# Kernel optimization log

Hardware: AMD Instinct MI355X
Metric: run time of the kernel (lower is better)

The kernel has to match this reference:

```python
import jax, jax.numpy as jnp
import numpy as np

VOX_X, VOX_Y, VOX_Z = 256, 256, 20   # ceil((pc_range[3:]-pc_range[:3]) / 0.4)
OUT_H, OUT_W, OUT_Z = 200, 200, 16   # hard-coded F.interpolate target in forward
C = 80                               # out_channels; sparse feat dim must match for concat
N_PTS = 200000
BS = 1
EPS = 1e-5


def _lin_interp(x, axis, out_size):
    """1D linear interp along `axis`, matching torch align_corners=False."""
    in_size = x.shape[axis]
    pos = (jnp.arange(out_size, dtype=jnp.float32) + 0.5) * (in_size / out_size) - 0.5
    pos = jnp.clip(pos, 0.0, in_size - 1)
    i0 = jnp.floor(pos).astype(jnp.int32)
    i1 = jnp.minimum(i0 + 1, in_size - 1)
    w = pos - i0.astype(jnp.float32)
    x0 = jnp.take(x, i0, axis=axis)
    x1 = jnp.take(x, i1, axis=axis)
    wshape = [1] * x.ndim
    wshape[axis] = out_size
    w = w.reshape(wshape)
    return x0 * (1.0 - w) + x1 * w


def setup_inputs() -> dict:
    key = jax.random.key(0)
    ks = jax.random.split(key, 8)
    bev_feats = jax.random.normal(ks[0], (BS, C, OUT_H, OUT_W, OUT_Z), dtype=jnp.float32)
    # coords: [batch_idx, x, y, z] with per-column valid ranges
    cb = jax.random.randint(ks[1], (N_PTS, 1), 0, BS, dtype=jnp.int32)
    cx = jax.random.randint(ks[2], (N_PTS, 1), 0, VOX_X, dtype=jnp.int32)
    cy = jax.random.randint(ks[3], (N_PTS, 1), 0, VOX_Y, dtype=jnp.int32)
    cz = jax.random.randint(ks[4], (N_PTS, 1), 0, VOX_Z, dtype=jnp.int32)
    coords = jnp.concatenate([cb, cx, cy, cz], axis=1)
    feats = jax.random.normal(ks[5], (N_PTS, C), dtype=jnp.float32)
    w_conv = jax.random.normal(ks[6], (C, 2 * C), dtype=jnp.float32) * (1.0 / np.sqrt(2 * C))
    b_conv = jnp.zeros((C,), dtype=jnp.float32)
    return {
        "bev_feats": bev_feats, "coords": coords, "feats": feats,
        "w_conv": w_conv, "b_conv": b_conv,
        "bn_gamma": jnp.ones((C,), jnp.float32), "bn_beta": jnp.zeros((C,), jnp.float32),
        "bn_mean": jnp.zeros((C,), jnp.float32), "bn_var": jnp.ones((C,), jnp.float32),
    }


def reference(bev_feats, coords, feats, w_conv, b_conv, bn_gamma, bn_beta, bn_mean, bn_var):
    bs = bev_feats.shape[0]
    voxel = jnp.zeros((bs, VOX_X, VOX_Y, VOX_Z, C), dtype=jnp.float32)
    voxel = voxel.at[coords[:, 0], coords[:, 1], coords[:, 2], coords[:, 3]].set(feats)
    # permute(0,4,2,1,3): (bs, X, Y, Z, C) -> (bs, C, Y, X, Z)
    prior = jnp.transpose(voxel, (0, 4, 2, 1, 3))
    # trilinear interpolate (256,256,20) -> (200,200,16), align_corners=False (separable)
    prior = _lin_interp(prior, 2, OUT_H)
    prior = _lin_interp(prior, 3, OUT_W)
    prior = _lin_interp(prior, 4, OUT_Z)
    # concat on channels -> 1x1x1 conv3d -> BN (eval stats) -> residual -> ReLU
    x = jnp.concatenate([bev_feats, prior], axis=1)  # (bs, 2C, H, W, Z)
    y = jnp.einsum('bchwz,oc->bohwz', x, w_conv) + b_conv[None, :, None, None, None]
    inv = bn_gamma * jax.lax.rsqrt(bn_var + EPS)
    y = y * inv[None, :, None, None, None] + (bn_beta - bn_mean * inv)[None, :, None, None, None]
    return jax.nn.relu(y + bev_feats)
```

## Files before the change

kernel.cpp:

```cpp
#include <hip/hip_runtime.h>
#include <hip/hip_bf16.h>

#define VXX 256
#define VYY 256
#define VZZ 20
#define NC  80
#define OH  200
#define OW  200
#define OZ  16
#define SPATIAL (OH*OW*OZ)
#define NVOX (VXX*VYY*VZZ)
#define EPSV 1e-5f
#define NS 64
#define NWG (SPATIAL/NS)
#define X_FOOT 6
#define NCELL (2*X_FOOT*VZZ)
#define SLOTS 48
#define PSTR 72
#define RSB 80
#define RSP 88

typedef float  f32x4 __attribute__((ext_vector_type(4)));
typedef short  s16x8 __attribute__((ext_vector_type(8)));

__device__ __forceinline__ ushort f2bf(float f) {
    uint u = __builtin_bit_cast(uint, f);
    u += 0x7FFFu + ((u >> 16) & 1u);
    return (ushort)(u >> 16);
}

__device__ __forceinline__ void bar_lgkm() {
    asm volatile("s_waitcnt lgkmcnt(0)" ::: "memory");
    __builtin_amdgcn_s_barrier();
    asm volatile("" ::: "memory");
}

__global__ void scatter_k(const int* __restrict__ coords, int npts,
                          int* __restrict__ winner) {
    int i = blockIdx.x * 256 + threadIdx.x;
    if (i >= npts) return;
    int b = coords[i*4+0];
    int x = coords[i*4+1];
    int y = coords[i*4+2];
    int z = coords[i*4+3];
    int vi = ((b*VXX + x)*VYY + y)*VZZ + z;
    atomicMax(&winner[vi], i);
}

__global__ void setup_k(const float* __restrict__ wconv,
                        const float* __restrict__ bconv,
                        const float* __restrict__ gamma,
                        const float* __restrict__ beta,
                        const float* __restrict__ mean,
                        const float* __restrict__ var,
                        int4* __restrict__ winner4,
                        ushort* __restrict__ wfrag,
                        float2* __restrict__ bnss) {
    const int b = blockIdx.x, tid = threadIdx.x;
    if (b < 1280) {
        winner4[b*256 + tid] = make_int4(-1, -1, -1, -1);
    } else if (b < 1330) {
        int idx = (b - 1280)*256 + tid;
        int f   = idx >> 9;
        int rem = idx & 511;
        int l   = rem >> 3;
        int j   = rem & 7;
        int mt  = f / 5;
        int ks  = f - mt*5;
        int o   = mt*16 + (l & 15);
        int c   = ks*32 + (l >> 4)*8 + j;
        wfrag[idx] = f2bf(wconv[o*160 + c]);
    } else if (tid < NC) {
        float inv = gamma[tid] * rsqrtf(var[tid] + EPSV);
        bnss[tid] = make_float2(inv, bconv[tid]*inv + beta[tid] - mean[tid]*inv);
    }
}

__launch_bounds__(256, 5)
__global__ void fused_k(const float* __restrict__ bev,
                        const float* __restrict__ feats,
                        const int*  __restrict__ winner,
                        const ushort* __restrict__ wfrag,
                        const float2* __restrict__ bnss,
                        float* __restrict__ out) {
    __shared__ __align__(16) ushort xb_lds[NS * RSB];
    __shared__ __align__(16) char   u_lds[20736];
    __shared__ int    idx_lds[NCELL];
    __shared__ int    slot_pi[SLOTS];
    __shared__ int    wavecnt[4];
    ushort* const P_lds  = (ushort*)u_lds;
    ushort* const Rt_lds = (ushort*)(u_lds + 9216);
    ushort* const xp_lds = (ushort*)u_lds;

    const int tid   = threadIdx.x;
    const int bid   = blockIdx.x;
    const int swzb  = (bid & 7) * (NWG/8) + (bid >> 3);
    const int sbase = swzb * NS;
    const int sl    = tid & 63;
    const int quarter = tid >> 6;
    const int wv    = quarter, lane = sl;

    const int h  = sbase / (OW * OZ);
    const int w0 = (sbase >> 4) % OW;
    float posy = (h + 0.5f) * ((float)VYY/(float)OH) - 0.5f;
    posy = fminf(fmaxf(posy, 0.f), (float)(VYY-1));
    const int   y0 = (int)posy;
    const int   y1 = min(y0+1, VYY-1);
    const float fy = posy - (float)y0;
    float posx0 = (w0 + 0.5f) * ((float)VXX/(float)OW) - 0.5f;
    posx0 = fminf(fmaxf(posx0, 0.f), (float)(VXX-1));
    const int xmin = (int)posx0;

    const int zq = sl & 15;
    const int wq = w0 + (sl >> 4);
    float posx = (wq + 0.5f) * ((float)VXX/(float)OW) - 0.5f;
    posx = fminf(fmaxf(posx, 0.f), (float)(VXX-1));
    const int   x0 = (int)posx;
    const int   x1 = min(x0+1, VXX-1);
    const float fxw = posx - (float)x0;
    float posz = (zq + 0.5f) * ((float)VZZ/(float)OZ) - 0.5f;
    posz = fminf(fmaxf(posz, 0.f), (float)(VZZ-1));
    const int   z0 = (int)posz;
    const int   z1 = min(z0+1, VZZ-1);
    const float fzw = posz - (float)z0;
    const int fx0 = x0 - xmin, fx1 = x1 - xmin;

    int pi = -1;
    if (tid < NCELL) {
        int fz  = tid % VZZ;
        int fx  = (tid / VZZ) % X_FOOT;
        int fyc = tid / (VZZ * X_FOOT);
        int xx  = min(xmin + fx, VXX-1);
        int yy  = fyc ? y1 : y0;
        pi = winner[(xx*VYY + yy)*VZZ + fz];
    }
    __builtin_amdgcn_sched_barrier(0);

    const int S = sbase + sl;
    float bvv[20];
    #pragma unroll
    for (int j = 0; j < 20; ++j)
        bvv[j] = bev[(quarter*20 + j)*SPATIAL + S];
    __builtin_amdgcn_sched_barrier(0);

    {
        uint* pz = (uint*)u_lds;
        #pragma unroll
        for (int i = 0; i < 9; ++i) pz[tid + i*256] = 0;
    }

    unsigned long long bm = __ballot(pi >= 0);
    if (lane == 0) wavecnt[wv] = __popcll(bm);
    bar_lgkm();
    int base = 0, nstot = 0;
    #pragma unroll
    for (int w2 = 0; w2 < 4; ++w2) {
        int c2 = wavecnt[w2];
        if (w2 < wv) base += c2;
        nstot += c2;
    }
    if (tid < NCELL) {
        int v = -1;
        if (pi >= 0) {
            int slot = base + __popcll(bm & ((1ull << lane) - 1ull));
            if (slot < SLOTS) { slot_pi[slot] = pi; v = slot; }
            else v = -(pi + 2);
        }
        idx_lds[tid] = v;
    }
    bar_lgkm();
    const int nst = min(nstot, SLOTS);

    const float4* feats4 = (const float4*)feats;
    const int myslot = tid >> 2, part = tid & 3;
    const bool rowact = (myslot < nst);
    float4 rbuf[5];
    if (rowact) {
        const float4* p = feats4 + slot_pi[myslot]*20 + part*5;
        #pragma unroll
        for (int q = 0; q < 5; ++q) rbuf[q] = p[q];
    }

    {
        const int ky = quarter >> 1, kx = quarter & 1;
        const float ywp = ky ? fy : 1.f - fy;
        const bool xdup = (fx1 == fx0);
        if (!(xdup && kx)) {
            const int   xf = kx ? fx1 : fx0;
            const float xw = xdup ? 1.f : (kx ? fxw : 1.f - fxw);
            #pragma unroll
            for (int kz = 0; kz < 2; ++kz) {
                int cell = (ky*X_FOOT + xf)*VZZ + (kz ? z1 : z0);
                int v = idx_lds[cell];
                if (v >= 0)
                    P_lds[sl*PSTR + v] = f2bf(ywp * xw * (kz ? fzw : 1.f - fzw));
            }
        }
    }

    #pragma unroll
    for (int j5 = 0; j5 < 5; ++j5) {
        ushort4 pk = make_ushort4(f2bf(bvv[j5*4+0]), f2bf(bvv[j5*4+1]),
                                  f2bf(bvv[j5*4+2]), f2bf(bvv[j5*4+3]));
        *(ushort4*)&xb_lds[sl*RSB + quarter*20 + j5*4] = pk;
    }

    {
        ushort vals[20];
        #pragma unroll
        for (int q = 0; q < 5; ++q) {
            vals[4*q+0] = rowact ? f2bf(rbuf[q].x) : (ushort)0;
            vals[4*q+1] = rowact ? f2bf(rbuf[q].y) : (ushort)0;
            vals[4*q+2] = rowact ? f2bf(rbuf[q].z) : (ushort)0;
            vals[4*q+3] = rowact ? f2bf(rbuf[q].w) : (ushort)0;
        }
        #pragma unroll
        for (int e = 0; e < 20; ++e)
            Rt_lds[(part*20 + e)*PSTR + myslot] = vals[e];
    }
    bar_lgkm();

    const int lrow = lane & 15, lgrp = lane >> 4;
    f32x4 pa[5];
    {
        const int prow = (wv*16 + lrow)*PSTR;
        s16x8 p0 = *(const s16x8*)&P_lds[prow +      lgrp*8];
        s16x8 p1 = *(const s16x8*)&P_lds[prow + 32 + lgrp*8];
        #pragma unroll
        for (int mt = 0; mt < 5; ++mt) {
            const int arow = (mt*16 + lrow)*PSTR;
            s16x8 a0 = *(const s16x8*)&Rt_lds[arow +      lgrp*8];
            s16x8 a1 = *(const s16x8*)&Rt_lds[arow + 32 + lgrp*8];
            pa[mt] = (f32x4){0.f, 0.f, 0.f, 0.f};
            pa[mt] = __builtin_amdgcn_mfma_f32_16x16x32_bf16(a0, p0, pa[mt], 0, 0, 0);
            pa[mt] = __builtin_amdgcn_mfma_f32_16x16x32_bf16(a1, p1, pa[mt], 0, 0, 0);
        }
    }
    bar_lgkm();
    #pragma unroll
    for (int mt = 0; mt < 5; ++mt) {
        ushort4 pk = make_ushort4(f2bf(pa[mt][0]), f2bf(pa[mt][1]),
                                  f2bf(pa[mt][2]), f2bf(pa[mt][3]));
        *(ushort4*)&xp_lds[(wv*16 + lrow)*RSP + mt*16 + lgrp*4] = pk;
    }

    if (nstot > SLOTS) {
        bar_lgkm();
        float add20[20];
        #pragma unroll
        for (int j = 0; j < 20; ++j) add20[j] = 0.f;
        bool any = false;
        #pragma unroll
        for (int k = 0; k < 8; ++k) {
            int kz = k & 1, kx = (k>>1)&1, ky = k>>2;
            int cell = (ky*X_FOOT + (kx ? fx1 : fx0))*VZZ + (kz ? z1 : z0);
            int v = idx_lds[cell];
            if (v < -1) {
                any = true;
                float wtk = (ky?fy:1.f-fy) * (kx?fxw:1.f-fxw) * (kz?fzw:1.f-fzw);
                const float4* p = feats4 + (-v - 2)*20 + quarter*5;
                #pragma unroll
                for (int q = 0; q < 5; ++q) {
                    float4 f = p[q];
                    add20[4*q]   += wtk*f.x; add20[4*q+1] += wtk*f.y;
                    add20[4*q+2] += wtk*f.z; add20[4*q+3] += wtk*f.w;
                }
            }
        }
        if (any) {
            #pragma unroll
            for (int q = 0; q < 5; ++q) {
                ushort* dst = &xp_lds[sl*RSP + quarter*20 + q*4];
                ushort4 old = *(ushort4*)dst;
                const ushort ov[4] = {old.x, old.y, old.z, old.w};
                ushort nv[4];
                #pragma unroll
                for (int e = 0; e < 4; ++e) {
                    float f = __builtin_bit_cast(float, (uint)ov[e] << 16) + add20[4*q+e];
                    nv[e] = f2bf(f);
                }
                *(ushort4*)dst = make_ushort4(nv[0], nv[1], nv[2], nv[3]);
            }
        }
    }
    bar_lgkm();

    f32x4 acc[5];
    #pragma unroll
    for (int mt = 0; mt < 5; ++mt) acc[mt] = (f32x4){0.f, 0.f, 0.f, 0.f};

    const int srow_b = (wv*16 + lrow) * RSB;
    const int srow_p = (wv*16 + lrow) * RSP;

    #pragma unroll
    for (int ks = 0; ks < 5; ++ks) {
        int c = ks*32 + lgrp*8;
        const ushort* bp = (c < 80) ? &xb_lds[srow_b + c]
                                    : &xp_lds[srow_p + (c - 80)];
        s16x8 b = *(const s16x8*)bp;
        #pragma unroll
        for (int mt = 0; mt < 5; ++mt) {
            s16x8 a = *(const s16x8*)&wfrag[((mt*5 + ks)*64 + lane)*8];
            acc[mt] = __builtin_amdgcn_mfma_f32_16x16x32_bf16(a, b, acc[mt], 0, 0, 0);
        }
    }

    const int slocal = wv*16 + lrow;
    const int sglob  = sbase + slocal;
    #pragma unroll
    for (int mt = 0; mt < 5; ++mt) {
        ushort4 rr = *(const ushort4*)&xb_lds[slocal*RSB + mt*16 + lgrp*4];
        const ushort rrv[4] = {rr.x, rr.y, rr.z, rr.w};
        #pragma unroll
        for (int r = 0; r < 4; ++r) {
            int o = mt*16 + lgrp*4 + r;
            float2 ss = bnss[o];
            float resid = __builtin_bit_cast(float, (uint)rrv[r] << 16);
            float v = acc[mt][r]*ss.x + ss.y + resid;
            out[o*SPATIAL + sglob] = fmaxf(v, 0.f);
        }
    }
}

extern "C" void kernel_launch(void* const* d_in, const int* in_sizes, int n_in,
                              void* d_out, int out_size, void* d_ws, size_t ws_size,
                              hipStream_t stream) {
    const float* bev    = (const float*)d_in[0];
    const int*   coords = (const int*)  d_in[1];
    const float* feats  = (const float*)d_in[2];
    const float* wconv  = (const float*)d_in[3];
    const float* bconv  = (const float*)d_in[4];
    const float* gamma  = (const float*)d_in[5];
    const float* beta   = (const float*)d_in[6];
    const float* mean   = (const float*)d_in[7];
    const float* var    = (const float*)d_in[8];
    float*       out    = (float*)d_out;

    int*    winner = (int*)d_ws;
    ushort* wfrag  = (ushort*)((char*)d_ws + (size_t)NVOX*4);
    float2* bnss   = (float2*)((char*)d_ws + (size_t)NVOX*4 + 25600);
    int npts = in_sizes[1] / 4;

    hipLaunchKernelGGL(setup_k, dim3(1331), dim3(256), 0, stream,
                       wconv, bconv, gamma, beta, mean, var,
                       (int4*)winner, wfrag, bnss);
    hipLaunchKernelGGL(scatter_k, dim3((npts + 255)/256), dim3(256), 0, stream,
                       coords, npts, winner);
    hipLaunchKernelGGL(fused_k, dim3(NWG), dim3(256), 0, stream,
                       bev, feats, winner, wfrag, bnss, out);
}
```

Measured before the change: 151.2 us.

## Make fused kernel persistent over 5 tiles with software-prefetched loads

The fused kernel now launches 2000 blocks, each looping over 5 consecutive 64-voxel tiles, instead of one tile per block. The next tile's winner indices and bev values are loaded into registers while the current tile's conv MFMAs and stores proceed, to hide global load latency and amortise per-block setup. The cost is more live registers, which may reduce occupancy under the 5-wave launch bound, and fewer blocks to spread across CUs, leaving some tail imbalance.

```diff
diff --git a/kernel.cpp b/kernel.cpp
--- a/kernel.cpp
+++ b/kernel.cpp
@@ -12,7 +12,8 @@
 #define NVOX (VXX*VYY*VZZ)
 #define EPSV 1e-5f
 #define NS 64
-#define NWG (SPATIAL/NS)
+#define NT 5
+#define NB 2000
 #define X_FOOT 6
 #define NCELL (2*X_FOOT*VZZ)
 #define SLOTS 48
@@ -92,232 +93,271 @@
     ushort* const Rt_lds = (ushort*)(u_lds + 9216);
     ushort* const xp_lds = (ushort*)u_lds;
 
-    const int tid   = threadIdx.x;
-    const int bid   = blockIdx.x;
-    const int swzb  = (bid & 7) * (NWG/8) + (bid >> 3);
-    const int sbase = swzb * NS;
-    const int sl    = tid & 63;
+    const int tid  = threadIdx.x;
+    const int sl   = tid & 63;
     const int quarter = tid >> 6;
-    const int wv    = quarter, lane = sl;
-
-    const int h  = sbase / (OW * OZ);
-    const int w0 = (sbase >> 4) % OW;
+    const int wv   = quarter, lane = sl;
+    const int lrow = lane & 15, lgrp = lane >> 4;
+
+    const int bid      = blockIdx.x;
+    const int xcd      = bid & 7, rank = bid >> 3;
+    const int tilebase = xcd*(NB/8*NT) + rank*NT;
+
+    const int h   = tilebase / 50;
+    const int w0b = (tilebase % 50) * 4;
+    const float XS = (float)VXX / (float)OW;
+
     float posy = (h + 0.5f) * ((float)VYY/(float)OH) - 0.5f;
     posy = fminf(fmaxf(posy, 0.f), (float)(VYY-1));
     const int   y0 = (int)posy;
     const int   y1 = min(y0+1, VYY-1);
     const float fy = posy - (float)y0;
-    float posx0 = (w0 + 0.5f) * ((float)VXX/(float)OW) - 0.5f;
-    posx0 = fminf(fmaxf(posx0, 0.f), (float)(VXX-1));
-    const int xmin = (int)posx0;
 
     const int zq = sl & 15;
-    const int wq = w0 + (sl >> 4);
-    float posx = (wq + 0.5f) * ((float)VXX/(float)OW) - 0.5f;
-    posx = fminf(fmaxf(posx, 0.f), (float)(VXX-1));
-    const int   x0 = (int)posx;
-    const int   x1 = min(x0+1, VXX-1);
-    const float fxw = posx - (float)x0;
     float posz = (zq + 0.5f) * ((float)VZZ/(float)OZ) - 0.5f;
     posz = fminf(fmaxf(posz, 0.f), (float)(VZZ-1));
     const int   z0 = (int)posz;
     const int   z1 = min(z0+1, VZZ-1);
     const float fzw = posz - (float)z0;
-    const int fx0 = x0 - xmin, fx1 = x1 - xmin;
-
-    int pi = -1;
-    if (tid < NCELL) {
-        int fz  = tid % VZZ;
-        int fx  = (tid / VZZ) % X_FOOT;
-        int fyc = tid / (VZZ * X_FOOT);
-        int xx  = min(xmin + fx, VXX-1);
-        int yy  = fyc ? y1 : y0;
-        pi = winner[(xx*VYY + yy)*VZZ + fz];
+
+    const int dfz  = tid % VZZ;
+    const int dfx  = (tid / VZZ) % X_FOOT;
+    const int dfyc = tid / (VZZ * X_FOOT);
+    const int dyy  = dfyc ? y1 : y0;
+
+    const float4* feats4 = (const float4*)feats;
+
+    int   pi = -1;
+    float bvv[20];
+    {
+        float px0 = (w0b + 0.5f)*XS - 0.5f;
+        px0 = fminf(fmaxf(px0, 0.f), (float)(VXX-1));
+        int xmin0 = (int)px0;
+        if (tid < NCELL) {
+            int xx = min(xmin0 + dfx, VXX-1);
+            pi = winner[(xx*VYY + dyy)*VZZ + dfz];
+        }
     }
     __builtin_amdgcn_sched_barrier(0);
-
-    const int S = sbase + sl;
-    float bvv[20];
-    #pragma unroll
-    for (int j = 0; j < 20; ++j)
-        bvv[j] = bev[(quarter*20 + j)*SPATIAL + S];
+    {
+        int S0 = tilebase*NS + sl;
+        #pragma unroll
+        for (int j = 0; j < 20; ++j)
+            bvv[j] = bev[(quarter*20 + j)*SPATIAL + S0];
+    }
     __builtin_amdgcn_sched_barrier(0);
-
     {
         uint* pz = (uint*)u_lds;
         #pragma unroll
         for (int i = 0; i < 9; ++i) pz[tid + i*256] = 0;
     }
 
-    unsigned long long bm = __ballot(pi >= 0);
-    if (lane == 0) wavecnt[wv] = __popcll(bm);
-    bar_lgkm();
-    int base = 0, nstot = 0;
     #pragma unroll
-    for (int w2 = 0; w2 < 4; ++w2) {
-        int c2 = wavecnt[w2];
-        if (w2 < wv) base += c2;
-        nstot += c2;
-    }
-    if (tid < NCELL) {
-        int v = -1;
-        if (pi >= 0) {
-            int slot = base + __popcll(bm & ((1ull << lane) - 1ull));
-            if (slot < SLOTS) { slot_pi[slot] = pi; v = slot; }
-            else v = -(pi + 2);
-        }
-        idx_lds[tid] = v;
-    }
-    bar_lgkm();
-    const int nst = min(nstot, SLOTS);
-
-    const float4* feats4 = (const float4*)feats;
-    const int myslot = tid >> 2, part = tid & 3;
-    const bool rowact = (myslot < nst);
-    float4 rbuf[5];
-    if (rowact) {
-        const float4* p = feats4 + slot_pi[myslot]*20 + part*5;
-        #pragma unroll
-        for (int q = 0; q < 5; ++q) rbuf[q] = p[q];
-    }
-
-    {
-        const int ky = quarter >> 1, kx = quarter & 1;
-        const float ywp = ky ? fy : 1.f - fy;
-        const bool xdup = (fx1 == fx0);
-        if (!(xdup && kx)) {
-            const int   xf = kx ? fx1 : fx0;
-            const float xw = xdup ? 1.f : (kx ? fxw : 1.f - fxw);
-            #pragma unroll
-            for (int kz = 0; kz < 2; ++kz) {
-                int cell = (ky*X_FOOT + xf)*VZZ + (kz ? z1 : z0);
+    for (int t = 0; t < NT; ++t) {
+        const int tile  = tilebase + t;
+        const int sbase = tile * NS;
+        const int w0    = w0b + 4*t;
+
+        float posx = (w0 + (sl >> 4) + 0.5f)*XS - 0.5f;
+        posx = fminf(fmaxf(posx, 0.f), (float)(VXX-1));
+        const int   x0 = (int)posx;
+        const int   x1 = min(x0+1, VXX-1);
+        const float fxw = posx - (float)x0;
+        float px0 = (w0 + 0.5f)*XS - 0.5f;
+        px0 = fminf(fmaxf(px0, 0.f), (float)(VXX-1));
+        const int xmin = (int)px0;
+        const int fx0 = x0 - xmin, fx1 = x1 - xmin;
+
+        unsigned long long bm = __ballot(pi >= 0);
+        if (lane == 0) wavecnt[wv] = __popcll(bm);
+        bar_lgkm();
+        int base = 0, nstot = 0;
+        #pragma unroll
+        for (int w2 = 0; w2 < 4; ++w2) {
+            int c2 = wavecnt[w2];
+            if (w2 < wv) base += c2;
+            nstot += c2;
+        }
+        if (tid < NCELL) {
+            int v = -1;
+            if (pi >= 0) {
+                int slot = base + __popcll(bm & ((1ull << lane) - 1ull));
+                if (slot < SLOTS) { slot_pi[slot] = pi; v = slot; }
+                else v = -(pi + 2);
+            }
+            idx_lds[tid] = v;
+        }
+        bar_lgkm();
+        const int nst = min(nstot, SLOTS);
+
+        const int myslot = tid >> 2, part = tid & 3;
+        const bool rowact = (myslot < nst);
+        float4 rbuf[5];
+        if (rowact) {
+            const float4* p = feats4 + slot_pi[myslot]*20 + part*5;
+            #pragma unroll
+            for (int q = 0; q < 5; ++q) rbuf[q] = p[q];
+        }
+
+        {
+            const int ky = quarter >> 1, kx = quarter & 1;
+            const float ywp = ky ? fy : 1.f - fy;
+            const bool xdup = (fx1 == fx0);
+            if (!(xdup && kx)) {
+                const int   xf = kx ? fx1 : fx0;
+                const float xw = xdup ? 1.f : (kx ? fxw : 1.f - fxw);
+                #pragma unroll
+                for (int kz = 0; kz < 2; ++kz) {
+                    int cell = (ky*X_FOOT + xf)*VZZ + (kz ? z1 : z0);
+                    int v = idx_lds[cell];
+                    if (v >= 0)
+                        P_lds[sl*PSTR + v] = f2bf(ywp * xw * (kz ? fzw : 1.f - fzw));
+                }
+            }
+        }
+
+        #pragma unroll
+        for (int j5 = 0; j5 < 5; ++j5) {
+            ushort4 pk = make_ushort4(f2bf(bvv[j5*4+0]), f2bf(bvv[j5*4+1]),
+                                      f2bf(bvv[j5*4+2]), f2bf(bvv[j5*4+3]));
+            *(ushort4*)&xb_lds[sl*RSB + quarter*20 + j5*4] = pk;
+        }
+
+        {
+            ushort vals[20];
+            #pragma unroll
+            for (int q = 0; q < 5; ++q) {
+                vals[4*q+0] = rowact ? f2bf(rbuf[q].x) : (ushort)0;
+                vals[4*q+1] = rowact ? f2bf(rbuf[q].y) : (ushort)0;
+                vals[4*q+2] = rowact ? f2bf(rbuf[q].z) : (ushort)0;
+                vals[4*q+3] = rowact ? f2bf(rbuf[q].w) : (ushort)0;
+            }
+            #pragma unroll
+            for (int e = 0; e < 20; ++e)
+                Rt_lds[(part*20 + e)*PSTR + myslot] = vals[e];
+        }
+        bar_lgkm();
+
+        f32x4 pa[5];
+        {
+            const int prow = (wv*16 + lrow)*PSTR;
+            s16x8 p0 = *(const s16x8*)&P_lds[prow +      lgrp*8];
+            s16x8 p1 = *(const s16x8*)&P_lds[prow + 32 + lgrp*8];
+            #pragma unroll
+            for (int mt = 0; mt < 5; ++mt) {
+                const int arow = (mt*16 + lrow)*PSTR;
+                s16x8 a0 = *(const s16x8*)&Rt_lds[arow +      lgrp*8];
+                s16x8 a1 = *(const s16x8*)&Rt_lds[arow + 32 + lgrp*8];
+                pa[mt] = (f32x4){0.f, 0.f, 0.f, 0.f};
+                pa[mt] = __builtin_amdgcn_mfma_f32_16x16x32_bf16(a0, p0, pa[mt], 0, 0, 0);
+                pa[mt] = __builtin_amdgcn_mfma_f32_16x16x32_bf16(a1, p1, pa[mt], 0, 0, 0);
+            }
+        }
+        bar_lgkm();
+        #pragma unroll
+        for (int mt = 0; mt < 5; ++mt) {
+            ushort4 pk = make_ushort4(f2bf(pa[mt][0]), f2bf(pa[mt][1]),
+                                      f2bf(pa[mt][2]), f2bf(pa[mt][3]));
+            *(ushort4*)&xp_lds[(wv*16 + lrow)*RSP + mt*16 + lgrp*4] = pk;
+        }
+
+        if (t + 1 < NT) {
+            float px0n = (w0 + 4 + 0.5f)*XS - 0.5f;
+            px0n = fminf(fmaxf(px0n, 0.f), (float)(VXX-1));
+            int xminN = (int)px0n;
+            pi = -1;
+            if (tid < NCELL) {
+                int xx = min(xminN + dfx, VXX-1);
+                pi = winner[(xx*VYY + dyy)*VZZ + dfz];
+            }
+            int Sn = (tile + 1)*NS + sl;
+            #pragma unroll
+            for (int j = 0; j < 20; ++j)
+                bvv[j] = bev[(quarter*20 + j)*SPATIAL + Sn];
+            __builtin_amdgcn_sched_barrier(0);
+        }
+
+        if (nstot > SLOTS) {
+            bar_lgkm();
+            float add20[20];
+            #pragma unroll
+            for (int j = 0; j < 20; ++j) add20[j] = 0.f;
+            bool any = false;
+            #pragma unroll
+            for (int k = 0; k < 8; ++k) {
+                int kz = k & 1, kx = (k>>1)&1, ky = k>>2;
+                int cell = (ky*X_FOOT + (kx ? fx1 : fx0))*VZZ + (kz ? z1 : z0);
                 int v = idx_lds[cell];
-                if (v >= 0)
-                    P_lds[sl*PSTR + v] = f2bf(ywp * xw * (kz ? fzw : 1.f - fzw));
-            }
-        }
-    }
-
-    #pragma unroll
-    for (int j5 = 0; j5 < 5; ++j5) {
-        ushort4 pk = make_ushort4(f2bf(bvv[j5*4+0]), f2bf(bvv[j5*4+1]),
-                                  f2bf(bvv[j5*4+2]), f2bf(bvv[j5*4+3]));
-        *(ushort4*)&xb_lds[sl*RSB + quarter*20 + j5*4] = pk;
-    }
-
-    {
-        ushort vals[20];
-        #pragma unroll
-        for (int q = 0; q < 5; ++q) {
-            vals[4*q+0] = rowact ? f2bf(rbuf[q].x) : (ushort)0;
-            vals[4*q+1] = rowact ? f2bf(rbuf[q].y) : (ushort)0;
-            vals[4*q+2] = rowact ? f2bf(rbuf[q].z) : (ushort)0;
-            vals[4*q+3] = rowact ? f2bf(rbuf[q].w) : (ushort)0;
-        }
-        #pragma unroll
-        for (int e = 0; e < 20; ++e)
-            Rt_lds[(part*20 + e)*PSTR + myslot] = vals[e];
-    }
-    bar_lgkm();
-
-    const int lrow = lane & 15, lgrp = lane >> 4;
-    f32x4 pa[5];
-    {
-        const int prow = (wv*16 + lrow)*PSTR;
-        s16x8 p0 = *(const s16x8*)&P_lds[prow +      lgrp*8];
-        s16x8 p1 = *(const s16x8*)&P_lds[prow + 32 + lgrp*8];
-        #pragma unroll
-        for (int mt = 0; mt < 5; ++mt) {
-            const int arow = (mt*16 + lrow)*PSTR;
-            s16x8 a0 = *(const s16x8*)&Rt_lds[arow +      lgrp*8];
-            s16x8 a1 = *(const s16x8*)&Rt_lds[arow + 32 + lgrp*8];
-            pa[mt] = (f32x4){0.f, 0.f, 0.f, 0.f};
-            pa[mt] = __builtin_amdgcn_mfma_f32_16x16x32_bf16(a0, p0, pa[mt], 0, 0, 0);
-            pa[mt] = __builtin_amdgcn_mfma_f32_16x16x32_bf16(a1, p1, pa[mt], 0, 0, 0);
-        }
-    }
-    bar_lgkm();
-    #pragma unroll
-    for (int mt = 0; mt < 5; ++mt) {
-        ushort4 pk = make_ushort4(f2bf(pa[mt][0]), f2bf(pa[mt][1]),
-                                  f2bf(pa[mt][2]), f2bf(pa[mt][3]));
-        *(ushort4*)&xp_lds[(wv*16 + lrow)*RSP + mt*16 + lgrp*4] = pk;
-    }
-
-    if (nstot > SLOTS) {
-        bar_lgkm();
-        float add20[20];
-        #pragma unroll
-        for (int j = 0; j < 20; ++j) add20[j] = 0.f;
-        bool any = false;
-        #pragma unroll
-        for (int k = 0; k < 8; ++k) {
-            int kz = k & 1, kx = (k>>1)&1, ky = k>>2;
-            int cell = (ky*X_FOOT + (kx ? fx1 : fx0))*VZZ + (kz ? z1 : z0);
-            int v = idx_lds[cell];
-            if (v < -1) {
-                any = true;
-                float wtk = (ky?fy:1.f-fy) * (kx?fxw:1.f-fxw) * (kz?fzw:1.f-fzw);
-                const float4* p = feats4 + (-v - 2)*20 + quarter*5;
+                if (v < -1) {
+                    any = true;
+                    float wtk = (ky?fy:1.f-fy) * (kx?fxw:1.f-fxw) * (kz?fzw:1.f-fzw);
+                    const float4* p = feats4 + (-v - 2)*20 + quarter*5;
+                    #pragma unroll
+                    for (int q = 0; q < 5; ++q) {
+                        float4 f = p[q];
+                        add20[4*q]   += wtk*f.x; add20[4*q+1] += wtk*f.y;
+                        add20[4*q+2] += wtk*f.z; add20[4*q+3] += wtk*f.w;
+                    }
+                }
+            }
+            if (any) {
                 #pragma unroll
                 for (int q = 0; q < 5; ++q) {
-                    float4 f = p[q];
-                    add20[4*q]   += wtk*f.x; add20[4*q+1] += wtk*f.y;
-                    add20[4*q+2] += wtk*f.z; add20[4*q+3] += wtk*f.w;
+                    ushort* dst = &xp_lds[sl*RSP + quarter*20 + q*4];
+                    ushort4 old = *(ushort4*)dst;
+                    const ushort ov[4] = {old.x, old.y, old.z, old.w};
+                    ushort nv[4];
+                    #pragma unroll
+                    for (int e = 0; e < 4; ++e) {
+                        float f = __builtin_bit_cast(float, (uint)ov[e] << 16) + add20[4*q+e];
+                        nv[e] = f2bf(f);
+                    }
+                    *(ushort4*)dst = make_ushort4(nv[0], nv[1], nv[2], nv[3]);
                 }
             }
         }
-        if (any) {
-            #pragma unroll
-            for (int q = 0; q < 5; ++q) {
-                ushort* dst = &xp_lds[sl*RSP + quarter*20 + q*4];
-                ushort4 old = *(ushort4*)dst;
-                const ushort ov[4] = {old.x, old.y, old.z, old.w};
-                ushort nv[4];
-                #pragma unroll
-                for (int e = 0; e < 4; ++e) {
-                    float f = __builtin_bit_cast(float, (uint)ov[e] << 16) + add20[4*q+e];
-                    nv[e] = f2bf(f);
-                }
-                *(ushort4*)dst = make_ushort4(nv[0], nv[1], nv[2], nv[3]);
-            }
-        }
-    }
-    bar_lgkm();
-
-    f32x4 acc[5];
-    #pragma unroll
-    for (int mt = 0; mt < 5; ++mt) acc[mt] = (f32x4){0.f, 0.f, 0.f, 0.f};
-
-    const int srow_b = (wv*16 + lrow) * RSB;
-    const int srow_p = (wv*16 + lrow) * RSP;
-
-    #pragma unroll
-    for (int ks = 0; ks < 5; ++ks) {
-        int c = ks*32 + lgrp*8;
-        const ushort* bp = (c < 80) ? &xb_lds[srow_b + c]
-                                    : &xp_lds[srow_p + (c - 80)];
-        s16x8 b = *(const s16x8*)bp;
+        bar_lgkm();
+
+        f32x4 acc[5];
+        #pragma unroll
+        for (int mt = 0; mt < 5; ++mt) acc[mt] = (f32x4){0.f, 0.f, 0.f, 0.f};
+
+        const int srow_b = (wv*16 + lrow) * RSB;
+        const int srow_p = (wv*16 + lrow) * RSP;
+
+        #pragma unroll
+        for (int ks = 0; ks < 5; ++ks) {
+            int c = ks*32 + lgrp*8;
+            const ushort* bp = (c < 80) ? &xb_lds[srow_b + c]
+                                        : &xp_lds[srow_p + (c - 80)];
+            s16x8 b = *(const s16x8*)bp;
+            #pragma unroll
+            for (int mt = 0; mt < 5; ++mt) {
+                s16x8 a = *(const s16x8*)&wfrag[((mt*5 + ks)*64 + lane)*8];
+                acc[mt] = __builtin_amdgcn_mfma_f32_16x16x32_bf16(a, b, acc[mt], 0, 0, 0);
+            }
+        }
+        bar_lgkm();
+
+        if (t + 1 < NT) {
+            uint* pz = (uint*)u_lds;
+            #pragma unroll
+            for (int i = 0; i < 9; ++i) pz[tid + i*256] = 0;
+        }
+        const int slocal = wv*16 + lrow;
+        const int sglob  = sbase + slocal;
         #pragma unroll
         for (int mt = 0; mt < 5; ++mt) {
-            s16x8 a = *(const s16x8*)&wfrag[((mt*5 + ks)*64 + lane)*8];
-            acc[mt] = __builtin_amdgcn_mfma_f32_16x16x32_bf16(a, b, acc[mt], 0, 0, 0);
-        }
-    }
-
-    const int slocal = wv*16 + lrow;
-    const int sglob  = sbase + slocal;
-    #pragma unroll
-    for (int mt = 0; mt < 5; ++mt) {
-        ushort4 rr = *(const ushort4*)&xb_lds[slocal*RSB + mt*16 + lgrp*4];
-        const ushort rrv[4] = {rr.x, rr.y, rr.z, rr.w};
-        #pragma unroll
-        for (int r = 0; r < 4; ++r) {
-            int o = mt*16 + lgrp*4 + r;
-            float2 ss = bnss[o];
-            float resid = __builtin_bit_cast(float, (uint)rrv[r] << 16);
-            float v = acc[mt][r]*ss.x + ss.y + resid;
-            out[o*SPATIAL + sglob] = fmaxf(v, 0.f);
+            ushort4 rr = *(const ushort4*)&xb_lds[slocal*RSB + mt*16 + lgrp*4];
+            const ushort rrv[4] = {rr.x, rr.y, rr.z, rr.w};
+            #pragma unroll
+            for (int r = 0; r < 4; ++r) {
+                int o = mt*16 + lgrp*4 + r;
+                float2 ss = bnss[o];
+                float resid = __builtin_bit_cast(float, (uint)rrv[r] << 16);
+                float v = acc[mt][r]*ss.x + ss.y + resid;
+                out[o*SPATIAL + sglob] = fmaxf(v, 0.f);
+            }
         }
     }
 }
@@ -346,6 +386,6 @@
                        (int4*)winner, wfrag, bnss);
     hipLaunchKernelGGL(scatter_k, dim3((npts + 255)/256), dim3(256), 0, stream,
                        coords, npts, winner);
-    hipLaunchKernelGGL(fused_k, dim3(NWG), dim3(256), 0, stream,
+    hipLaunchKernelGGL(fused_k, dim3(NB), dim3(256), 0, stream,
                        bev, feats, winner, wfrag, bnss, out);
 }
```

New measurement: 463.2 us. 3.06x slower.

## Load bev directly into MFMA B-fragments and reload fp32 residual, drop xb LDS

Applied to the files above, without the earlier changes.

Removes the xb_lds staging buffer. Each lane now loads the bev channels it needs straight into registers already laid out as MFMA B fragments, instead of writing them to shared memory and reading them back. The residual is reloaded from global memory in fp32 rather than taken from the bf16 copy in LDS, which also makes the residual more precise. This cuts shared memory use (possibly allowing higher occupancy) and LDS traffic, at the cost of a second global read of bev (mostly cache hits) and more registers.

```diff
diff --git a/kernel.cpp b/kernel.cpp
--- a/kernel.cpp
+++ b/kernel.cpp
@@ -17,7 +17,6 @@
 #define NCELL (2*X_FOOT*VZZ)
 #define SLOTS 48
 #define PSTR 72
-#define RSB 80
 #define RSP 88
 
 typedef float  f32x4 __attribute__((ext_vector_type(4)));
@@ -83,11 +82,10 @@
                         const ushort* __restrict__ wfrag,
                         const float2* __restrict__ bnss,
                         float* __restrict__ out) {
-    __shared__ __align__(16) ushort xb_lds[NS * RSB];
-    __shared__ __align__(16) char   u_lds[20736];
-    __shared__ int    idx_lds[NCELL];
-    __shared__ int    slot_pi[SLOTS];
-    __shared__ int    wavecnt[4];
+    __shared__ __align__(16) char u_lds[20736];
+    __shared__ int idx_lds[NCELL];
+    __shared__ int slot_pi[SLOTS];
+    __shared__ int wavecnt[4];
     ushort* const P_lds  = (ushort*)u_lds;
     ushort* const Rt_lds = (ushort*)(u_lds + 9216);
     ushort* const xp_lds = (ushort*)u_lds;
@@ -99,6 +97,8 @@
     const int sl    = tid & 63;
     const int quarter = tid >> 6;
     const int wv    = quarter, lane = sl;
+    const int lrow  = lane & 15, lgrp = lane >> 4;
+    const int srow  = wv*16 + lrow;
 
     const int h  = sbase / (OW * OZ);
     const int w0 = (sbase >> 4) % OW;
@@ -136,11 +136,16 @@
     }
     __builtin_amdgcn_sched_barrier(0);
 
-    const int S = sbase + sl;
-    float bvv[20];
-    #pragma unroll
-    for (int j = 0; j < 20; ++j)
-        bvv[j] = bev[(quarter*20 + j)*SPATIAL + S];
+    float bfv[24];
+    #pragma unroll
+    for (int kk = 0; kk < 3; ++kk) {
+        int c0 = kk*32 + lgrp*8;
+        if (c0 < 80) {
+            #pragma unroll
+            for (int j = 0; j < 8; ++j)
+                bfv[kk*8 + j] = bev[(c0 + j)*SPATIAL + sbase + srow];
+        }
+    }
     __builtin_amdgcn_sched_barrier(0);
 
     {
@@ -198,13 +203,6 @@
         }
     }
 
-    #pragma unroll
-    for (int j5 = 0; j5 < 5; ++j5) {
-        ushort4 pk = make_ushort4(f2bf(bvv[j5*4+0]), f2bf(bvv[j5*4+1]),
-                                  f2bf(bvv[j5*4+2]), f2bf(bvv[j5*4+3]));
-        *(ushort4*)&xb_lds[sl*RSB + quarter*20 + j5*4] = pk;
-    }
-
     {
         ushort vals[20];
         #pragma unroll
@@ -220,10 +218,9 @@
     }
     bar_lgkm();
 
-    const int lrow = lane & 15, lgrp = lane >> 4;
     f32x4 pa[5];
     {
-        const int prow = (wv*16 + lrow)*PSTR;
+        const int prow = srow*PSTR;
         s16x8 p0 = *(const s16x8*)&P_lds[prow +      lgrp*8];
         s16x8 p1 = *(const s16x8*)&P_lds[prow + 32 + lgrp*8];
         #pragma unroll
@@ -241,8 +238,30 @@
     for (int mt = 0; mt < 5; ++mt) {
         ushort4 pk = make_ushort4(f2bf(pa[mt][0]), f2bf(pa[mt][1]),
                                   f2bf(pa[mt][2]), f2bf(pa[mt][3]));
-        *(ushort4*)&xp_lds[(wv*16 + lrow)*RSP + mt*16 + lgrp*4] = pk;
-    }
+        *(ushort4*)&xp_lds[srow*RSP + mt*16 + lgrp*4] = pk;
+    }
+
+    s16x8 bfrag[3];
+    #pragma unroll
+    for (int kk = 0; kk < 3; ++kk) {
+        int c0 = kk*32 + lgrp*8;
+        if (c0 < 80) {
+            s16x8 t;
+            #pragma unroll
+            for (int j = 0; j < 8; ++j) t[j] = (short)f2bf(bfv[kk*8 + j]);
+            bfrag[kk] = t;
+        } else {
+            bfrag[kk] = (s16x8){0,0,0,0,0,0,0,0};
+        }
+    }
+
+    float resv[20];
+    #pragma unroll
+    for (int mt = 0; mt < 5; ++mt)
+        #pragma unroll
+        for (int r = 0; r < 4; ++r)
+            resv[mt*4 + r] = bev[(mt*16 + lgrp*4 + r)*SPATIAL + sbase + srow];
+    __builtin_amdgcn_sched_barrier(0);
 
     if (nstot > SLOTS) {
         bar_lgkm();
@@ -289,15 +308,19 @@
     #pragma unroll
     for (int mt = 0; mt < 5; ++mt) acc[mt] = (f32x4){0.f, 0.f, 0.f, 0.f};
 
-    const int srow_b = (wv*16 + lrow) * RSB;
-    const int srow_p = (wv*16 + lrow) * RSP;
+    const int srow_p = srow * RSP;
 
     #pragma unroll
     for (int ks = 0; ks < 5; ++ks) {
-        int c = ks*32 + lgrp*8;
-        const ushort* bp = (c < 80) ? &xb_lds[srow_b + c]
-                                    : &xp_lds[srow_p + (c - 80)];
-        s16x8 b = *(const s16x8*)bp;
+        s16x8 b;
+        if (ks < 2) {
+            b = bfrag[ks];
+        } else if (ks == 2) {
+            if (lgrp < 2) b = bfrag[2];
+            else          b = *(const s16x8*)&xp_lds[srow_p + (lgrp*8 - 16)];
+        } else {
+            b = *(const s16x8*)&xp_lds[srow_p + (ks*32 + lgrp*8 - 80)];
+        }
         #pragma unroll
         for (int mt = 0; mt < 5; ++mt) {
             s16x8 a = *(const s16x8*)&wfrag[((mt*5 + ks)*64 + lane)*8];
@@ -305,18 +328,14 @@
         }
     }
 
-    const int slocal = wv*16 + lrow;
-    const int sglob  = sbase + slocal;
+    const int sglob = sbase + srow;
     #pragma unroll
     for (int mt = 0; mt < 5; ++mt) {
-        ushort4 rr = *(const ushort4*)&xb_lds[slocal*RSB + mt*16 + lgrp*4];
-        const ushort rrv[4] = {rr.x, rr.y, rr.z, rr.w};
         #pragma unroll
         for (int r = 0; r < 4; ++r) {
             int o = mt*16 + lgrp*4 + r;
             float2 ss = bnss[o];
-            float resid = __builtin_bit_cast(float, (uint)rrv[r] << 16);
-            float v = acc[mt][r]*ss.x + ss.y + resid;
+            float v = acc[mt][r]*ss.x + ss.y + resv[mt*4 + r];
             out[o*SPATIAL + sglob] = fmaxf(v, 0.f);
         }
     }
```

Result: slower. 317.0 us (+109.7%).

## Split voxel-slot discovery into a separate kernel ahead of fused conv

Applied to the files above, without the earlier changes.

Adds a discovery kernel that, for each 64-voxel output tile, looks up winner indices in its footprint, compacts them into slots and writes per-tile counts, slot point indices and 8-bit cell-to-slot maps to workspace. The fused kernel then reads these precomputed tables instead of doing the winner lookups, ballot and block reductions itself. This shortens the dependent chain before the feature and bev loads and removes some barriers and LDS use. In exchange it adds a kernel launch and extra global traffic, and it only runs when the workspace is large enough, otherwise it falls back to the original kernel.

```diff
diff --git a/kernel.cpp b/kernel.cpp
--- a/kernel.cpp
+++ b/kernel.cpp
@@ -19,6 +19,14 @@
 #define PSTR 72
 #define RSB 80
 #define RSP 88
+#define DTPB 4
+
+#define WS_WFRAG  5242880
+#define WS_BNSS   5268480
+#define WS_CNT    5269120
+#define WS_SLOTPI 5309120
+#define WS_IDX8   7229120
+#define WS_NEED   9789120
 
 typedef float  f32x4 __attribute__((ext_vector_type(4)));
 typedef short  s16x8 __attribute__((ext_vector_type(8)));
@@ -76,13 +84,284 @@
     }
 }
 
+__global__ void disc_k(const int* __restrict__ winner,
+                       int* __restrict__ cnt_g,
+                       int* __restrict__ slotpi_g,
+                       signed char* __restrict__ idx8_g) {
+    __shared__ int wavecnt[4];
+    const int tid = threadIdx.x;
+    const int wv = tid >> 6, lane = tid & 63;
+    for (int tt = 0; tt < DTPB; ++tt) {
+        const int tile  = blockIdx.x * DTPB + tt;
+        const int sbase = tile * NS;
+        const int h  = sbase / (OW * OZ);
+        const int w0 = (sbase >> 4) % OW;
+        float posy = (h + 0.5f) * ((float)VYY/(float)OH) - 0.5f;
+        posy = fminf(fmaxf(posy, 0.f), (float)(VYY-1));
+        int y0 = (int)posy, y1 = min(y0+1, VYY-1);
+        float posx0 = (w0 + 0.5f) * ((float)VXX/(float)OW) - 0.5f;
+        posx0 = fminf(fmaxf(posx0, 0.f), (float)(VXX-1));
+        int xmin = (int)posx0;
+
+        int pi = -1;
+        if (tid < NCELL) {
+            int fz  = tid % VZZ;
+            int fx  = (tid / VZZ) % X_FOOT;
+            int fyc = tid / (VZZ * X_FOOT);
+            int xx  = min(xmin + fx, VXX-1);
+            int yy  = fyc ? y1 : y0;
+            pi = winner[(xx*VYY + yy)*VZZ + fz];
+        }
+        unsigned long long bm = __ballot(pi >= 0);
+        if (lane == 0) wavecnt[wv] = __popcll(bm);
+        __syncthreads();
+        int base = 0, nstot = 0;
+        #pragma unroll
+        for (int w2 = 0; w2 < 4; ++w2) {
+            int c2 = wavecnt[w2];
+            if (w2 < wv) base += c2;
+            nstot += c2;
+        }
+        if (tid < NCELL) {
+            signed char v8 = -1;
+            if (pi >= 0) {
+                int slot = base + __popcll(bm & ((1ull << lane) - 1ull));
+                if (slot < SLOTS) { slotpi_g[tile*SLOTS + slot] = pi; v8 = (signed char)slot; }
+                else v8 = -2;
+            }
+            idx8_g[tile*256 + tid] = v8;
+        }
+        if (tid == 0) cnt_g[tile] = nstot;
+        __syncthreads();
+    }
+}
+
 __launch_bounds__(256, 5)
-__global__ void fused_k(const float* __restrict__ bev,
-                        const float* __restrict__ feats,
-                        const int*  __restrict__ winner,
-                        const ushort* __restrict__ wfrag,
-                        const float2* __restrict__ bnss,
-                        float* __restrict__ out) {
+__global__ void fused_split(const float* __restrict__ bev,
+                            const float* __restrict__ feats,
+                            const int*  __restrict__ winner,
+                            const ushort* __restrict__ wfrag,
+                            const float2* __restrict__ bnss,
+                            const int* __restrict__ cnt_g,
+                            const int* __restrict__ slotpi_g,
+                            const signed char* __restrict__ idx8_g,
+                            float* __restrict__ out) {
+    __shared__ __align__(16) ushort xb_lds[NS * RSB];
+    __shared__ __align__(16) char   u_lds[20736];
+    ushort* const P_lds  = (ushort*)u_lds;
+    ushort* const Rt_lds = (ushort*)(u_lds + 9216);
+    ushort* const xp_lds = (ushort*)u_lds;
+
+    const int tid   = threadIdx.x;
+    const int bid   = blockIdx.x;
+    const int swzb  = (bid & 7) * (NWG/8) + (bid >> 3);
+    const int tile  = swzb;
+    const int sbase = swzb * NS;
+    const int sl    = tid & 63;
+    const int quarter = tid >> 6;
+    const int wv    = quarter, lane = sl;
+    const int lrow  = lane & 15, lgrp = lane >> 4;
+    const int srow  = wv*16 + lrow;
+
+    const int h  = sbase / (OW * OZ);
+    const int w0 = (sbase >> 4) % OW;
+    float posy = (h + 0.5f) * ((float)VYY/(float)OH) - 0.5f;
+    posy = fminf(fmaxf(posy, 0.f), (float)(VYY-1));
+    const int   y0 = (int)posy;
+    const int   y1 = min(y0+1, VYY-1);
+    const float fy = posy - (float)y0;
+    float posx0 = (w0 + 0.5f) * ((float)VXX/(float)OW) - 0.5f;
+    posx0 = fminf(fmaxf(posx0, 0.f), (float)(VXX-1));
+    const int xmin = (int)posx0;
+
+    const int zq = sl & 15;
+    const int wq = w0 + (sl >> 4);
+    float posx = (wq + 0.5f) * ((float)VXX/(float)OW) - 0.5f;
+    posx = fminf(fmaxf(posx, 0.f), (float)(VXX-1));
+    const int   x0 = (int)posx;
+    const int   x1 = min(x0+1, VXX-1);
+    const float fxw = posx - (float)x0;
+    float posz = (zq + 0.5f) * ((float)VZZ/(float)OZ) - 0.5f;
+    posz = fminf(fmaxf(posz, 0.f), (float)(VZZ-1));
+    const int   z0 = (int)posz;
+    const int   z1 = min(z0+1, VZZ-1);
+    const float fzw = posz - (float)z0;
+    const int fx0 = x0 - xmin, fx1 = x1 - xmin;
+
+    const int nstot = cnt_g[tile];
+    const int myslot = tid >> 2, part = tid & 3;
+    const int spi = slotpi_g[tile*SLOTS + (myslot < SLOTS ? myslot : 0)];
+    const int ky = quarter >> 1, kx = quarter & 1;
+    const bool xdup = (fx1 == fx0);
+    const int xf = kx ? fx1 : fx0;
+    const int cellA = (ky*X_FOOT + xf)*VZZ + z0;
+    const int cellB = (ky*X_FOOT + xf)*VZZ + z1;
+    const int vA = (int)idx8_g[tile*256 + cellA];
+    const int vB = (int)idx8_g[tile*256 + cellB];
+    __builtin_amdgcn_sched_barrier(0);
+
+    const float4* feats4 = (const float4*)feats;
+    const int nst = min(nstot, SLOTS);
+    const bool rowact = (myslot < nst);
+    float4 rbuf[5];
+    if (rowact) {
+        const float4* p = feats4 + spi*20 + part*5;
+        #pragma unroll
+        for (int q = 0; q < 5; ++q) rbuf[q] = p[q];
+    }
+    __builtin_amdgcn_sched_barrier(0);
+
+    const int S = sbase + sl;
+    float bvv[20];
+    #pragma unroll
+    for (int j = 0; j < 20; ++j)
+        bvv[j] = bev[(quarter*20 + j)*SPATIAL + S];
+    __builtin_amdgcn_sched_barrier(0);
+
+    {
+        uint* pz = (uint*)u_lds;
+        #pragma unroll
+        for (int i = 0; i < 9; ++i) pz[tid + i*256] = 0;
+    }
+    bar_lgkm();
+
+    if (!(xdup && kx)) {
+        const float ywp = ky ? fy : 1.f - fy;
+        const float xw  = xdup ? 1.f : (kx ? fxw : 1.f - fxw);
+        if (vA >= 0) P_lds[sl*PSTR + vA] = f2bf(ywp * xw * (1.f - fzw));
+        if (vB >= 0) P_lds[sl*PSTR + vB] = f2bf(ywp * xw * fzw);
+    }
+
+    {
+        ushort vals[20];
+        #pragma unroll
+        for (int q = 0; q < 5; ++q) {
+            vals[4*q+0] = rowact ? f2bf(rbuf[q].x) : (ushort)0;
+            vals[4*q+1] = rowact ? f2bf(rbuf[q].y) : (ushort)0;
+            vals[4*q+2] = rowact ? f2bf(rbuf[q].z) : (ushort)0;
+            vals[4*q+3] = rowact ? f2bf(rbuf[q].w) : (ushort)0;
+        }
+        #pragma unroll
+        for (int e = 0; e < 20; ++e)
+            Rt_lds[(part*20 + e)*PSTR + myslot] = vals[e];
+    }
+
+    #pragma unroll
+    for (int j5 = 0; j5 < 5; ++j5) {
+        ushort4 pk = make_ushort4(f2bf(bvv[j5*4+0]), f2bf(bvv[j5*4+1]),
+                                  f2bf(bvv[j5*4+2]), f2bf(bvv[j5*4+3]));
+        *(ushort4*)&xb_lds[sl*RSB + quarter*20 + j5*4] = pk;
+    }
+    bar_lgkm();
+
+    f32x4 pa[5];
+    {
+        const int prow = srow*PSTR;
+        s16x8 p0 = *(const s16x8*)&P_lds[prow +      lgrp*8];
+        s16x8 p1 = *(const s16x8*)&P_lds[prow + 32 + lgrp*8];
+        #pragma unroll
+        for (int mt = 0; mt < 5; ++mt) {
+            const int arow = (mt*16 + lrow)*PSTR;
+            s16x8 a0 = *(const s16x8*)&Rt_lds[arow +      lgrp*8];
+            s16x8 a1 = *(const s16x8*)&Rt_lds[arow + 32 + lgrp*8];
+            pa[mt] = (f32x4){0.f, 0.f, 0.f, 0.f};
+            pa[mt] = __builtin_amdgcn_mfma_f32_16x16x32_bf16(a0, p0, pa[mt], 0, 0, 0);
+            pa[mt] = __builtin_amdgcn_mfma_f32_16x16x32_bf16(a1, p1, pa[mt], 0, 0, 0);
+        }
+    }
+    bar_lgkm();
+    #pragma unroll
+    for (int mt = 0; mt < 5; ++mt) {
+        ushort4 pk = make_ushort4(f2bf(pa[mt][0]), f2bf(pa[mt][1]),
+                                  f2bf(pa[mt][2]), f2bf(pa[mt][3]));
+        *(ushort4*)&xp_lds[srow*RSP + mt*16 + lgrp*4] = pk;
+    }
+
+    if (nstot > SLOTS) {
+        bar_lgkm();
+        float add20[20];
+        #pragma unroll
+        for (int j = 0; j < 20; ++j) add20[j] = 0.f;
+        bool any = false;
+        #pragma unroll
+        for (int k = 0; k < 8; ++k) {
+            int kz = k & 1, kxx = (k>>1)&1, kyy = k>>2;
+            int cell = (kyy*X_FOOT + (kxx ? fx1 : fx0))*VZZ + (kz ? z1 : z0);
+            int v8 = (int)idx8_g[tile*256 + cell];
+            if (v8 == -2) {
+                any = true;
+                int pi2 = winner[(((kxx ? x1 : x0)*VYY) + (kyy ? y1 : y0))*VZZ + (kz ? z1 : z0)];
+                float wtk = (kyy?fy:1.f-fy) * (kxx?fxw:1.f-fxw) * (kz?fzw:1.f-fzw);
+                const float4* p = feats4 + pi2*20 + quarter*5;
+                #pragma unroll
+                for (int q = 0; q < 5; ++q) {
+                    float4 f = p[q];
+                    add20[4*q]   += wtk*f.x; add20[4*q+1] += wtk*f.y;
+                    add20[4*q+2] += wtk*f.z; add20[4*q+3] += wtk*f.w;
+                }
+            }
+        }
+        if (any) {
+            #pragma unroll
+            for (int q = 0; q < 5; ++q) {
+                ushort* dst = &xp_lds[sl*RSP + quarter*20 + q*4];
+                ushort4 old = *(ushort4*)dst;
+                const ushort ov[4] = {old.x, old.y, old.z, old.w};
+                ushort nv[4];
+                #pragma unroll
+                for (int e = 0; e < 4; ++e) {
+                    float f = __builtin_bit_cast(float, (uint)ov[e] << 16) + add20[4*q+e];
+                    nv[e] = f2bf(f);
+                }
+                *(ushort4*)dst = make_ushort4(nv[0], nv[1], nv[2], nv[3]);
+            }
+        }
+    }
+    bar_lgkm();
+
+    f32x4 acc[5];
+    #pragma unroll
+    for (int mt = 0; mt < 5; ++mt) acc[mt] = (f32x4){0.f, 0.f, 0.f, 0.f};
+
+    const int srow_b = srow * RSB;
+    const int srow_p = srow * RSP;
+
+    #pragma unroll
+    for (int ks = 0; ks < 5; ++ks) {
+        int c = ks*32 + lgrp*8;
+        const ushort* bp = (c < 80) ? &xb_lds[srow_b + c]
+                                    : &xp_lds[srow_p + (c - 80)];
+        s16x8 b = *(const s16x8*)bp;
+        #pragma unroll
+        for (int mt = 0; mt < 5; ++mt) {
+            s16x8 a = *(const s16x8*)&wfrag[((mt*5 + ks)*64 + lane)*8];
+            acc[mt] = __builtin_amdgcn_mfma_f32_16x16x32_bf16(a, b, acc[mt], 0, 0, 0);
+        }
+    }
+
+    const int sglob = sbase + srow;
+    #pragma unroll
+    for (int mt = 0; mt < 5; ++mt) {
+        ushort4 rr = *(const ushort4*)&xb_lds[srow_b + mt*16 + lgrp*4];
+        const ushort rrv[4] = {rr.x, rr.y, rr.z, rr.w};
+        #pragma unroll
+        for (int r = 0; r < 4; ++r) {
+            int o = mt*16 + lgrp*4 + r;
+            float2 ss = bnss[o];
+            float resid = __builtin_bit_cast(float, (uint)rrv[r] << 16);
+            float v = acc[mt][r]*ss.x + ss.y + resid;
+            out[o*SPATIAL + sglob] = fmaxf(v, 0.f);
+        }
+    }
+}
+
+__launch_bounds__(256, 5)
+__global__ void fused_mono(const float* __restrict__ bev,
+                           const float* __restrict__ feats,
+                           const int*  __restrict__ winner,
+                           const ushort* __restrict__ wfrag,
+                           const float2* __restrict__ bnss,
+                           float* __restrict__ out) {
     __shared__ __align__(16) ushort xb_lds[NS * RSB];
     __shared__ __align__(16) char   u_lds[20736];
     __shared__ int    idx_lds[NCELL];
@@ -99,6 +378,8 @@
     const int sl    = tid & 63;
     const int quarter = tid >> 6;
     const int wv    = quarter, lane = sl;
+    const int lrow  = lane & 15, lgrp = lane >> 4;
+    const int srow  = wv*16 + lrow;
 
     const int h  = sbase / (OW * OZ);
     const int w0 = (sbase >> 4) % OW;
@@ -220,10 +501,9 @@
     }
     bar_lgkm();
 
-    const int lrow = lane & 15, lgrp = lane >> 4;
     f32x4 pa[5];
     {
-        const int prow = (wv*16 + lrow)*PSTR;
+        const int prow = srow*PSTR;
         s16x8 p0 = *(const s16x8*)&P_lds[prow +      lgrp*8];
         s16x8 p1 = *(const s16x8*)&P_lds[prow + 32 + lgrp*8];
         #pragma unroll
@@ -241,7 +521,7 @@
     for (int mt = 0; mt < 5; ++mt) {
         ushort4 pk = make_ushort4(f2bf(pa[mt][0]), f2bf(pa[mt][1]),
                                   f2bf(pa[mt][2]), f2bf(pa[mt][3]));
-        *(ushort4*)&xp_lds[(wv*16 + lrow)*RSP + mt*16 + lgrp*4] = pk;
+        *(ushort4*)&xp_lds[srow*RSP + mt*16 + lgrp*4] = pk;
     }
 
     if (nstot > SLOTS) {
@@ -289,8 +569,8 @@
     #pragma unroll
     for (int mt = 0; mt < 5; ++mt) acc[mt] = (f32x4){0.f, 0.f, 0.f, 0.f};
 
-    const int srow_b = (wv*16 + lrow) * RSB;
-    const int srow_p = (wv*16 + lrow) * RSP;
+    const int srow_b = srow * RSB;
+    const int srow_p = srow * RSP;
 
     #pragma unroll
     for (int ks = 0; ks < 5; ++ks) {
@@ -305,11 +585,10 @@
         }
     }
 
-    const int slocal = wv*16 + lrow;
-    const int sglob  = sbase + slocal;
+    const int sglob = sbase + srow;
     #pragma unroll
     for (int mt = 0; mt < 5; ++mt) {
-        ushort4 rr = *(const ushort4*)&xb_lds[slocal*RSB + mt*16 + lgrp*4];
+        ushort4 rr = *(const ushort4*)&xb_lds[srow_b + mt*16 + lgrp*4];
         const ushort rrv[4] = {rr.x, rr.y, rr.z, rr.w};
         #pragma unroll
         for (int r = 0; r < 4; ++r) {
@@ -337,8 +616,8 @@
     float*       out    = (float*)d_out;
 
     int*    winner = (int*)d_ws;
-    ushort* wfrag  = (ushort*)((char*)d_ws + (size_t)NVOX*4);
-    float2* bnss   = (float2*)((char*)d_ws + (size_t)NVOX*4 + 25600);
+    ushort* wfrag  = (ushort*)((char*)d_ws + WS_WFRAG);
+    float2* bnss   = (float2*)((char*)d_ws + WS_BNSS);
     int npts = in_sizes[1] / 4;
 
     hipLaunchKernelGGL(setup_k, dim3(1331), dim3(256), 0, stream,
@@ -346,6 +625,18 @@
                        (int4*)winner, wfrag, bnss);
     hipLaunchKernelGGL(scatter_k, dim3((npts + 255)/256), dim3(256), 0, stream,
                        coords, npts, winner);
-    hipLaunchKernelGGL(fused_k, dim3(NWG), dim3(256), 0, stream,
-                       bev, feats, winner, wfrag, bnss, out);
-}
+
+    if (ws_size >= (size_t)WS_NEED) {
+        int*         cnt_g    = (int*)((char*)d_ws + WS_CNT);
+        int*         slotpi_g = (int*)((char*)d_ws + WS_SLOTPI);
+        signed char* idx8_g   = (signed char*)((char*)d_ws + WS_IDX8);
+        hipLaunchKernelGGL(disc_k, dim3(NWG/DTPB), dim3(256), 0, stream,
+                           winner, cnt_g, slotpi_g, idx8_g);
+        hipLaunchKernelGGL(fused_split, dim3(NWG), dim3(256), 0, stream,
+                           bev, feats, winner, wfrag, bnss,
+                           cnt_g, slotpi_g, idx8_g, out);
+    } else {
+        hipLaunchKernelGGL(fused_mono, dim3(NWG), dim3(256), 0, stream,
+                           bev, feats, winner, wfrag, bnss, out);
+    }
+}
```

Result: slower. 163.0 us (+7.8%).
